# Kernel tuning notes

Hardware: AMD Instinct MI355X
Metric: run time of the kernel (lower is better)

The kernel has to match this reference:

```python
import math
import jax, jax.numpy as jnp
import numpy as np

B, S, D = 4, 2048, 1024
EPS_LN = 1e-5
EPS_MAS = 1e-9


def layernorm(x, g, b):
    m = jnp.mean(x, axis=-1, keepdims=True)
    v = jnp.mean(jnp.square(x - m), axis=-1, keepdims=True)
    return (x - m) * jax.lax.rsqrt(v + EPS_LN) * g + b


def spl(x, proto_w, mu_w, mu_b, gate):
    # match_values = x @ proto^T / sqrt(d);  comp = silu(x @ mu^T + b)
    match = jnp.einsum('bsd,od->bso', x, proto_w) / math.sqrt(x.shape[-1])
    comp = jax.nn.silu(jnp.einsum('bsd,od->bso', x, mu_w) + mu_b)
    return comp, match, gate


def branch(comp, match, gate, passthrough):
    # mas_normalize on the 1-D gate vector (cost), broadcast over [B,S,D]
    cost = gate / (jnp.max(jnp.abs(gate)) + EPS_MAS)
    rl = match - cost
    mrl = jax.nn.relu(rl)
    mask = (rl > 0).astype(comp.dtype)
    return comp * mrl + passthrough * (1.0 - mask)


def causal_attention(q, k, v):
    # num_heads = 1, head_dim = D, is_causal=True
    scale = 1.0 / math.sqrt(q.shape[-1])
    scores = jnp.einsum('bqd,bkd->bqk', q, k) * scale
    causal = jnp.tril(jnp.ones((q.shape[1], k.shape[1]), dtype=bool))
    scores = jnp.where(causal, scores, jnp.asarray(-1e9, scores.dtype))
    p = jax.nn.softmax(scores, axis=-1)
    return jnp.einsum('bqk,bkd->bqd', p, v)


def setup_inputs() -> dict:
    key = jax.random.key(0)
    ks = jax.random.split(key, 16)
    d = D
    std = 0.02
    inp = {
        'x': jax.random.normal(ks[0], (B, S, d), jnp.float32),
        'ln_g': jnp.ones((d,), jnp.float32),
        'ln_b': jnp.zeros((d,), jnp.float32),
    }
    names = ['q', 'k', 'v', 'o']
    for i, n in enumerate(names):
        inp[f'{n}_mu_w'] = std * jax.random.normal(ks[1 + 3 * i], (d, d), jnp.float32)
        inp[f'{n}_mu_b'] = jnp.zeros((d,), jnp.float32)
        inp[f'{n}_proto'] = std * jax.random.normal(ks[2 + 3 * i], (d, d), jnp.float32)
        inp[f'{n}_gate'] = 0.1 * jax.random.normal(ks[3 + 3 * i], (d,), jnp.float32)
    return inp


def reference(x, ln_g, ln_b,
              q_mu_w, q_mu_b, q_proto, q_gate,
              k_mu_w, k_mu_b, k_proto, k_gate,
              v_mu_w, v_mu_b, v_proto, v_gate,
              o_mu_w, o_mu_b, o_proto, o_gate):
    ln1_out = layernorm(x, ln_g, ln_b)

    c_q, mv_q, g_q = spl(ln1_out, q_proto, q_mu_w, q_mu_b, q_gate)
    c_k, mv_k, g_k = spl(ln1_out, k_proto, k_mu_w, k_mu_b, k_gate)
    c_v, mv_v, g_v = spl(ln1_out, v_proto, v_mu_w, v_mu_b, v_gate)

    q = branch(c_q, mv_q, g_q, ln1_out)
    k = branch(c_k, mv_k, g_k, ln1_out)
    v = branch(c_v, mv_v, g_v, ln1_out)

    attn_out = causal_attention(q, k, v)

    c_o, mv_o, g_o = spl(attn_out, o_proto, o_mu_w, o_mu_b, o_gate)
    masked_o = branch(c_o, mv_o, g_o, attn_out)

    x_out = x + masked_o
    return x_out
```

## Files before the change

### kernel.cpp

```cpp
#include <hip/hip_runtime.h>
#include <hip/hip_bf16.h>
#include <cmath>
#include <cstdint>

typedef _Float16 f16;
typedef _Float16 f16x8 __attribute__((ext_vector_type(8)));
typedef float f32x4 __attribute__((ext_vector_type(4)));

#define D_ 1024
#define S_ 2048


__device__ __forceinline__ void gload_lds16(const void* g, void* l) {
  __builtin_amdgcn_global_load_lds(
      (const __attribute__((address_space(1))) void*)(unsigned long long)(uintptr_t)g,
      (__attribute__((address_space(3))) void*)(unsigned int)(uintptr_t)l,
      16, 0, 0);
}

__device__ __forceinline__ void stage_tile(const f16* __restrict__ src, int ld,
                                           f16* lds, int wid, int lane) {
  const int r = (wid << 5) + (lane >> 2);
  const int c = (lane & 3) ^ ((r >> 1) & 3);
  const f16* g0 = src + (size_t)r * ld + (c << 3);
  gload_lds16(g0, lds + (wid << 10));
  gload_lds16(g0 + (size_t)(ld << 4), lds + (wid << 10) + 512);
}

__device__ __forceinline__ int lds_off(int row, int cb) {
  return (row << 5) + ((cb ^ ((row >> 1) & 3)) << 3);
}

__device__ __forceinline__ void split1024(float v, f16& h, f16& l) {
  float s = v * 1024.f;
  h = (f16)s;
  l = (f16)(s - (float)h);
}

__global__ __launch_bounds__(256) void convert_w(
    const float* __restrict__ s0, const float* __restrict__ s1,
    const float* __restrict__ s2, const float* __restrict__ s3,
    const float* __restrict__ s4, const float* __restrict__ s5,
    const float* __restrict__ s6, const float* __restrict__ s7,
    f16* __restrict__ dst) {
  const float* srcs[8] = {s0, s1, s2, s3, s4, s5, s6, s7};
  const float* sp = srcs[blockIdx.y];
  f16* hi = dst + (size_t)blockIdx.y * 2097152;
  f16* lo = hi + 1048576;
  const int i = (blockIdx.x * 256 + threadIdx.x) << 2;
  float4 f = *(const float4*)(sp + i);
  __align__(8) f16 h4[4], l4[4];
  split1024(f.x, h4[0], l4[0]); split1024(f.y, h4[1], l4[1]);
  split1024(f.z, h4[2], l4[2]); split1024(f.w, h4[3], l4[3]);
  *(uint2*)(hi + i) = *(uint2*)h4;
  *(uint2*)(lo + i) = *(uint2*)l4;
}

__global__ __launch_bounds__(256) void cost_k(
    const float* __restrict__ g0, const float* __restrict__ g1,
    const float* __restrict__ g2, const float* __restrict__ g3,
    float* __restrict__ cost) {
  const float* gp = blockIdx.x == 0 ? g0 : blockIdx.x == 1 ? g1
                   : blockIdx.x == 2 ? g2 : g3;
  const int t = threadIdx.x;
  float4 v = *(const float4*)(gp + (t << 2));
  float mx = fmaxf(fmaxf(fabsf(v.x), fabsf(v.y)), fmaxf(fabsf(v.z), fabsf(v.w)));
  for (int o = 32; o; o >>= 1) mx = fmaxf(mx, __shfl_xor(mx, o, 64));
  __shared__ float red[4];
  if ((t & 63) == 0) red[t >> 6] = mx;
  __syncthreads();
  mx = fmaxf(fmaxf(red[0], red[1]), fmaxf(red[2], red[3]));
  const float den = mx + 1e-9f;
  float4 o = {v.x / den, v.y / den, v.z / den, v.w / den};
  *(float4*)(cost + (blockIdx.x << 10) + (t << 2)) = o;
}

__global__ __launch_bounds__(256) void layernorm_k(
    const float* __restrict__ x, const float* __restrict__ g,
    const float* __restrict__ bta, f16* __restrict__ Lh, f16* __restrict__ Ll) {
  const int row = blockIdx.x, t = threadIdx.x;
  const float* xr = x + (size_t)row * D_;
  float4 v = *(const float4*)(xr + (t << 2));
  float s = v.x + v.y + v.z + v.w;
  float q = v.x * v.x + v.y * v.y + v.z * v.z + v.w * v.w;
  for (int o = 32; o; o >>= 1) { s += __shfl_xor(s, o, 64); q += __shfl_xor(q, o, 64); }
  __shared__ float red[8];
  const int wid = t >> 6;
  if ((t & 63) == 0) { red[wid] = s; red[4 + wid] = q; }
  __syncthreads();
  s = red[0] + red[1] + red[2] + red[3];
  q = red[4] + red[5] + red[6] + red[7];
  const float mean = s * (1.f / D_);
  const float var = q * (1.f / D_) - mean * mean;
  const float inv = 1.f / sqrtf(var + 1e-5f);
  float4 gv = *(const float4*)(g + (t << 2));
  float4 bv = *(const float4*)(bta + (t << 2));
  __align__(8) f16 h4[4], l4[4];
  split1024((v.x - mean) * inv * gv.x + bv.x, h4[0], l4[0]);
  split1024((v.y - mean) * inv * gv.y + bv.y, h4[1], l4[1]);
  split1024((v.z - mean) * inv * gv.z + bv.z, h4[2], l4[2]);
  split1024((v.w - mean) * inv * gv.w + bv.w, h4[3], l4[3]);
  const size_t off = (size_t)row * D_ + (t << 2);
  *(uint2*)(Lh + off) = *(uint2*)h4;
  *(uint2*)(Ll + off) = *(uint2*)l4;
}

template <int EPI, int MUP>
__global__ __launch_bounds__(256, 2) void dual_gemm_branch(
    const f16* __restrict__ Ah, const f16* __restrict__ Al,
    const f16* __restrict__ Wph, const f16* __restrict__ Wpl,
    const f16* __restrict__ Wmh, const f16* __restrict__ Wml,
    const float* __restrict__ bias, const float* __restrict__ cost,
    const f16* __restrict__ passh, const f16* __restrict__ passl,
    const float* __restrict__ xres, f16* __restrict__ outh,
    f16* __restrict__ outl, float* __restrict__ outf) {
  __shared__ __align__(16) f16 lAh[4096], lAl[4096], lPh[4096], lPl[4096],
      lMh[4096], lMl[4096];
  const int tid = threadIdx.x, wid = tid >> 6, lane = tid & 63;
  const int row0 = blockIdx.x << 7, col0 = blockIdx.y << 7;
  const int wr = (wid >> 1) << 6, wc = (wid & 1) << 6;
  const int arow = lane & 15, cb = lane >> 4;
  const f32x4 zero = {0.f, 0.f, 0.f, 0.f};
  f32x4 accP[4][4], accM[4][4];
#pragma unroll
  for (int m = 0; m < 4; ++m)
#pragma unroll
    for (int n = 0; n < 4; ++n) { accP[m][n] = zero; accM[m][n] = zero; }
  const f16* Ahb = Ah + (size_t)row0 * D_;
  const f16* Alb = Al + (size_t)row0 * D_;
  const f16* Phb = Wph + (size_t)col0 * D_;
  const f16* Plb = Wpl + (size_t)col0 * D_;
  const f16* Mhb = Wmh + (size_t)col0 * D_;
  const f16* Mlb = Wml + (size_t)col0 * D_;
  for (int k = 0; k < D_; k += 32) {
    stage_tile(Ahb + k, D_, lAh, wid, lane);
    stage_tile(Alb + k, D_, lAl, wid, lane);
    stage_tile(Phb + k, D_, lPh, wid, lane);
    stage_tile(Plb + k, D_, lPl, wid, lane);
    stage_tile(Mhb + k, D_, lMh, wid, lane);
    stage_tile(Mlb + k, D_, lMl, wid, lane);
    __syncthreads();
    f16x8 bph[4], bpl[4], bmh[4], bml[4];
#pragma unroll
    for (int n = 0; n < 4; ++n) {
      const int bo = lds_off(wc + n * 16 + arow, cb);
      bph[n] = *(const f16x8*)&lPh[bo];
      bpl[n] = *(const f16x8*)&lPl[bo];
      bmh[n] = *(const f16x8*)&lMh[bo];
      bml[n] = *(const f16x8*)&lMl[bo];
    }
#pragma unroll
    for (int m = 0; m < 4; ++m) {
      const int ao = lds_off(wr + m * 16 + arow, cb);
      f16x8 ah = *(const f16x8*)&lAh[ao];
      f16x8 al = *(const f16x8*)&lAl[ao];
#pragma unroll
      for (int n = 0; n < 4; ++n) {
        accP[m][n] = __builtin_amdgcn_mfma_f32_16x16x32_f16(ah, bph[n], accP[m][n], 0, 0, 0);
        accP[m][n] = __builtin_amdgcn_mfma_f32_16x16x32_f16(ah, bpl[n], accP[m][n], 0, 0, 0);
        accP[m][n] = __builtin_amdgcn_mfma_f32_16x16x32_f16(al, bph[n], accP[m][n], 0, 0, 0);
        accM[m][n] = __builtin_amdgcn_mfma_f32_16x16x32_f16(ah, bmh[n], accM[m][n], 0, 0, 0);
        accM[m][n] = __builtin_amdgcn_mfma_f32_16x16x32_f16(ah, bml[n], accM[m][n], 0, 0, 0);
        if (MUP == 3)
          accM[m][n] = __builtin_amdgcn_mfma_f32_16x16x32_f16(al, bmh[n], accM[m][n], 0, 0, 0);
      }
    }
    __syncthreads();
  }
#pragma unroll
  for (int m = 0; m < 4; ++m) {
    const int rb = row0 + wr + m * 16 + ((lane >> 4) << 2);
#pragma unroll
    for (int n = 0; n < 4; ++n) {
      const int col = col0 + wc + n * 16 + (lane & 15);
      const float cb2 = cost[col], bb = bias[col];
#pragma unroll
      for (int j = 0; j < 4; ++j) {
        const size_t off = (size_t)(rb + j) * D_ + col;
        const float match = accP[m][n][j] * (1.f / 33554432.f);
        const float pre = accM[m][n][j] * (1.f / 1048576.f) + bb;
        const float comp = pre / (1.f + expf(-pre));
        const float rl = match - cb2;
        float ov;
        if (rl > 0.f) ov = comp * rl;
        else ov = ((float)passh[off] + (float)passl[off]) * (1.f / 1024.f);
        if (EPI == 0) {
          f16 h, l; split1024(ov, h, l);
          outh[off] = h; outl[off] = l;
        } else {
          outf[off] = xres[off] + ov;
        }
      }
    }
  }
}

__global__ __launch_bounds__(256) void transpose_v(
    const f16* __restrict__ Vh, const f16* __restrict__ Vl,
    f16* __restrict__ VTh, f16* __restrict__ VTl) {
  const int iz = blockIdx.z, b = iz & 3;
  const f16* src = (iz >> 2) ? Vl : Vh;
  f16* dst = (iz >> 2) ? VTl : VTh;
  const int d0 = blockIdx.x << 6, s0 = blockIdx.y << 6;
  __shared__ f16 tl[64][65];
  const int c = threadIdx.x & 63, r4 = threadIdx.x >> 6;
  const f16* vb = src + (size_t)b * S_ * D_;
#pragma unroll
  for (int i = 0; i < 16; ++i) {
    const int sr = (r4 << 4) + i;
    tl[sr][c] = vb[(size_t)(s0 + sr) * D_ + d0 + c];
  }
  __syncthreads();
  f16* db = dst + (size_t)b * D_ * S_;
#pragma unroll
  for (int i = 0; i < 16; ++i) {
    const int dr = (r4 << 4) + i;
    db[(size_t)(d0 + dr) * S_ + s0 + c] = tl[c][dr];
  }
}

__global__ __launch_bounds__(256, 2) void scores_gemm(
    const f16* __restrict__ Qh, const f16* __restrict__ Ql,
    const f16* __restrict__ Kh, const f16* __restrict__ Kl,
    float* __restrict__ SC) {
  const int rt = blockIdx.x, ct = blockIdx.y, b = blockIdx.z;
  if (ct > rt) return;
  __shared__ __align__(16) f16 lQh[4096], lQl[4096], lKh[4096], lKl[4096];
  const int tid = threadIdx.x, wid = tid >> 6, lane = tid & 63;
  const int row0 = rt << 7, col0 = ct << 7;
  const int wr = (wid >> 1) << 6, wc = (wid & 1) << 6;
  const int arow = lane & 15, cb = lane >> 4;
  const f32x4 zero = {0.f, 0.f, 0.f, 0.f};
  f32x4 acc[4][4];
#pragma unroll
  for (int m = 0; m < 4; ++m)
#pragma unroll
    for (int n = 0; n < 4; ++n) acc[m][n] = zero;
  const f16* Qhb = Qh + ((size_t)b * S_ + row0) * D_;
  const f16* Qlb = Ql + ((size_t)b * S_ + row0) * D_;
  const f16* Khb = Kh + ((size_t)b * S_ + col0) * D_;
  const f16* Klb = Kl + ((size_t)b * S_ + col0) * D_;
  for (int k = 0; k < D_; k += 32) {
    stage_tile(Qhb + k, D_, lQh, wid, lane);
    stage_tile(Qlb + k, D_, lQl, wid, lane);
    stage_tile(Khb + k, D_, lKh, wid, lane);
    stage_tile(Klb + k, D_, lKl, wid, lane);
    __syncthreads();
    f16x8 bh[4], bl[4];
#pragma unroll
    for (int n = 0; n < 4; ++n) {
      const int bo = lds_off(wc + n * 16 + arow, cb);
      bh[n] = *(const f16x8*)&lKh[bo];
      bl[n] = *(const f16x8*)&lKl[bo];
    }
#pragma unroll
    for (int m = 0; m < 4; ++m) {
      const int ao = lds_off(wr + m * 16 + arow, cb);
      f16x8 ah = *(const f16x8*)&lQh[ao];
      f16x8 al = *(const f16x8*)&lQl[ao];
#pragma unroll
      for (int n = 0; n < 4; ++n) {
        acc[m][n] = __builtin_amdgcn_mfma_f32_16x16x32_f16(ah, bh[n], acc[m][n], 0, 0, 0);
        acc[m][n] = __builtin_amdgcn_mfma_f32_16x16x32_f16(ah, bl[n], acc[m][n], 0, 0, 0);
        acc[m][n] = __builtin_amdgcn_mfma_f32_16x16x32_f16(al, bh[n], acc[m][n], 0, 0, 0);
      }
    }
    __syncthreads();
  }
  float* scb = SC + (size_t)b * S_ * S_;
#pragma unroll
  for (int m = 0; m < 4; ++m) {
    const int rb = row0 + wr + m * 16 + ((lane >> 4) << 2);
#pragma unroll
    for (int n = 0; n < 4; ++n) {
      const int col = col0 + wc + n * 16 + (lane & 15);
#pragma unroll
      for (int j = 0; j < 4; ++j)
        scb[(size_t)(rb + j) * S_ + col] = acc[m][n][j] * (1.f / 33554432.f);
    }
  }
}

__global__ __launch_bounds__(256) void softmax_rows(float* __restrict__ SC) {
  const int r = blockIdx.x;
  const int s = r & 2047;
  float* rowf = SC + (size_t)r * S_;
  const int t = threadIdx.x, c0 = t << 3;
  float f[8];
  float4 u0 = *(const float4*)(rowf + c0);
  float4 u1 = *(const float4*)(rowf + c0 + 4);
  f[0] = u0.x; f[1] = u0.y; f[2] = u0.z; f[3] = u0.w;
  f[4] = u1.x; f[5] = u1.y; f[6] = u1.z; f[7] = u1.w;
  float mx = -3.0e38f;
#pragma unroll
  for (int j = 0; j < 8; ++j)
    if (c0 + j <= s) mx = fmaxf(mx, f[j]);
  for (int o = 32; o; o >>= 1) mx = fmaxf(mx, __shfl_xor(mx, o, 64));
  __shared__ float red[8];
  const int wid = t >> 6;
  if ((t & 63) == 0) red[wid] = mx;
  __syncthreads();
  mx = fmaxf(fmaxf(red[0], red[1]), fmaxf(red[2], red[3]));
  float e[8];
  float sum = 0.f;
#pragma unroll
  for (int j = 0; j < 8; ++j) {
    e[j] = (c0 + j <= s) ? expf(f[j] - mx) : 0.f;
    sum += e[j];
  }
  for (int o = 32; o; o >>= 1) sum += __shfl_xor(sum, o, 64);
  if ((t & 63) == 0) red[4 + wid] = sum;
  __syncthreads();
  sum = red[4] + red[5] + red[6] + red[7];
  f16* rowh = (f16*)rowf;
  __align__(16) f16 ph[8], pl[8];
#pragma unroll
  for (int j = 0; j < 8; ++j) {
    float p = (e[j] / sum) * 2048.f;
    ph[j] = (f16)p;
    pl[j] = (f16)(p - (float)ph[j]);
  }
  *(uint4*)(rowh + c0) = *(uint4*)ph;
  *(uint4*)(rowh + 2048 + c0) = *(uint4*)pl;
}

__global__ __launch_bounds__(256, 2) void pv_gemm(
    const f16* __restrict__ P, const f16* __restrict__ VTh,
    const f16* __restrict__ VTl, f16* __restrict__ Ath, f16* __restrict__ Atl) {
  const int rt = blockIdx.x, ct = blockIdx.y, b = blockIdx.z;
  __shared__ __align__(16) f16 lPh[4096], lPl[4096], lVh[4096], lVl[4096];
  const int tid = threadIdx.x, wid = tid >> 6, lane = tid & 63;
  const int row0 = rt << 7, col0 = ct << 7;
  const int wr = (wid >> 1) << 6, wc = (wid & 1) << 6;
  const int arow = lane & 15, cb = lane >> 4;
  const f32x4 zero = {0.f, 0.f, 0.f, 0.f};
  f32x4 acc[4][4];
#pragma unroll
  for (int m = 0; m < 4; ++m)
#pragma unroll
    for (int n = 0; n < 4; ++n) acc[m][n] = zero;
  const f16* Pb = P + ((size_t)b * S_ + row0) * 4096;
  const f16* Vhb = VTh + (size_t)b * D_ * S_ + (size_t)col0 * S_;
  const f16* Vlb = VTl + (size_t)b * D_ * S_ + (size_t)col0 * S_;
  const int kend = (rt + 1) << 7;
  for (int k = 0; k < kend; k += 32) {
    stage_tile(Pb + k, 4096, lPh, wid, lane);
    stage_tile(Pb + 2048 + k, 4096, lPl, wid, lane);
    stage_tile(Vhb + k, S_, lVh, wid, lane);
    stage_tile(Vlb + k, S_, lVl, wid, lane);
    __syncthreads();
    f16x8 bh[4], bl[4];
#pragma unroll
    for (int n = 0; n < 4; ++n) {
      const int bo = lds_off(wc + n * 16 + arow, cb);
      bh[n] = *(const f16x8*)&lVh[bo];
      bl[n] = *(const f16x8*)&lVl[bo];
    }
#pragma unroll
    for (int m = 0; m < 4; ++m) {
      const int ao = lds_off(wr + m * 16 + arow, cb);
      f16x8 ah = *(const f16x8*)&lPh[ao];
      f16x8 al = *(const f16x8*)&lPl[ao];
#pragma unroll
      for (int n = 0; n < 4; ++n) {
        acc[m][n] = __builtin_amdgcn_mfma_f32_16x16x32_f16(ah, bh[n], acc[m][n], 0, 0, 0);
        acc[m][n] = __builtin_amdgcn_mfma_f32_16x16x32_f16(ah, bl[n], acc[m][n], 0, 0, 0);
        acc[m][n] = __builtin_amdgcn_mfma_f32_16x16x32_f16(al, bh[n], acc[m][n], 0, 0, 0);
      }
    }
    __syncthreads();
  }
#pragma unroll
  for (int m = 0; m < 4; ++m) {
    const int rb = row0 + wr + m * 16 + ((lane >> 4) << 2);
#pragma unroll
    for (int n = 0; n < 4; ++n) {
      const int col = col0 + wc + n * 16 + (lane & 15);
#pragma unroll
      for (int j = 0; j < 4; ++j) {
        const float at = acc[m][n][j] * (1.f / 2097152.f);
        const size_t off = ((size_t)b * S_ + rb + j) * D_ + col;
        f16 h, l; split1024(at, h, l);
        Ath[off] = h; Atl[off] = l;
      }
    }
  }
}

extern "C" void kernel_launch(void* const* d_in, const int* in_sizes, int n_in,
                              void* d_out, int out_size, void* d_ws, size_t ws_size,
                              hipStream_t stream) {
  (void)in_sizes; (void)n_in; (void)out_size; (void)ws_size;
  const float* x      = (const float*)d_in[0];
  const float* ln_g   = (const float*)d_in[1];
  const float* ln_b   = (const float*)d_in[2];
  const float* q_mu_w = (const float*)d_in[3];
  const float* q_mu_b = (const float*)d_in[4];
  const float* q_pro  = (const float*)d_in[5];
  const float* q_gate = (const float*)d_in[6];
  const float* k_mu_w = (const float*)d_in[7];
  const float* k_mu_b = (const float*)d_in[8];
  const float* k_pro  = (const float*)d_in[9];
  const float* k_gate = (const float*)d_in[10];
  const float* v_mu_w = (const float*)d_in[11];
  const float* v_mu_b = (const float*)d_in[12];
  const float* v_pro  = (const float*)d_in[13];
  const float* v_gate = (const float*)d_in[14];
  const float* o_mu_w = (const float*)d_in[15];
  const float* o_mu_b = (const float*)d_in[16];
  const float* o_pro  = (const float*)d_in[17];
  const float* o_gate = (const float*)d_in[18];

  char* w = (char*)d_ws;
  f16* WB = (f16*)w;
  const size_t WS = 2097152;
  f16* Lh  = (f16*)(w + 33554432);
  f16* Ll  = (f16*)(w + 50331648);
  f16* Qh  = (f16*)(w + 67108864);
  f16* Ql  = (f16*)(w + 83886080);
  f16* Kh  = (f16*)(w + 100663296);
  f16* Kl  = (f16*)(w + 117440512);
  f16* VTh = (f16*)(w + 134217728);
  f16* VTl = (f16*)(w + 150994944);
  float* SC = (float*)(w + 167772160);
  float* COST = (float*)(w + 234881024);
  f16* Vh = (f16*)SC;
  f16* Vl = (f16*)(w + 184549376);
  f16* Ath = Qh;  f16* Atl = Ql;

  convert_w<<<dim3(1024, 8), 256, 0, stream>>>(
      q_pro, q_mu_w, k_pro, k_mu_w, v_pro, v_mu_w, o_pro, o_mu_w, WB);
  cost_k<<<4, 256, 0, stream>>>(q_gate, k_gate, v_gate, o_gate, COST);
  layernorm_k<<<8192, 256, 0, stream>>>(x, ln_g, ln_b, Lh, Ll);

  dual_gemm_branch<0, 3><<<dim3(64, 8), 256, 0, stream>>>(
      Lh, Ll, WB, WB + 1048576, WB + WS, WB + WS + 1048576,
      q_mu_b, COST, Lh, Ll, nullptr, Qh, Ql, nullptr);
  dual_gemm_branch<0, 3><<<dim3(64, 8), 256, 0, stream>>>(
      Lh, Ll, WB + 2 * WS, WB + 2 * WS + 1048576, WB + 3 * WS, WB + 3 * WS + 1048576,
      k_mu_b, COST + 1024, Lh, Ll, nullptr, Kh, Kl, nullptr);
  dual_gemm_branch<0, 3><<<dim3(64, 8), 256, 0, stream>>>(
      Lh, Ll, WB + 4 * WS, WB + 4 * WS + 1048576, WB + 5 * WS, WB + 5 * WS + 1048576,
      v_mu_b, COST + 2048, Lh, Ll, nullptr, Vh, Vl, nullptr);

  transpose_v<<<dim3(16, 32, 8), 256, 0, stream>>>(Vh, Vl, VTh, VTl);
  scores_gemm<<<dim3(16, 16, 4), 256, 0, stream>>>(Qh, Ql, Kh, Kl, SC);
  softmax_rows<<<8192, 256, 0, stream>>>(SC);
  pv_gemm<<<dim3(16, 8, 4), 256, 0, stream>>>((const f16*)SC, VTh, VTl, Ath, Atl);

  dual_gemm_branch<1, 2><<<dim3(64, 8), 256, 0, stream>>>(
      Ath, Atl, WB + 6 * WS, WB + 6 * WS + 1048576, WB + 7 * WS, WB + 7 * WS + 1048576,
      o_mu_b, COST + 3072, Ath, Atl, x, nullptr, nullptr, (float*)d_out);
}
```

Measured before the change: 708.3 us.

## Double-buffer dual GEMM LDS loads and enlarge block tile to 256 rows

```diff
diff --git a/kernel.cpp b/kernel.cpp
--- a/kernel.cpp
+++ b/kernel.cpp
@@ -16,6 +16,16 @@
       (const __attribute__((address_space(1))) void*)(unsigned long long)(uintptr_t)g,
       (__attribute__((address_space(3))) void*)(unsigned int)(uintptr_t)l,
       16, 0, 0);
+}
+
+__device__ __forceinline__ int lds_off(int row, int cb) {
+  return (row << 5) + ((cb ^ ((row >> 1) & 3)) << 3);
+}
+
+__device__ __forceinline__ void split1024(float v, f16& h, f16& l) {
+  float s = v * 1024.f;
+  h = (f16)s;
+  l = (f16)(s - (float)h);
 }
 
 __device__ __forceinline__ void stage_tile(const f16* __restrict__ src, int ld,
@@ -25,16 +35,6 @@
   const f16* g0 = src + (size_t)r * ld + (c << 3);
   gload_lds16(g0, lds + (wid << 10));
   gload_lds16(g0 + (size_t)(ld << 4), lds + (wid << 10) + 512);
-}
-
-__device__ __forceinline__ int lds_off(int row, int cb) {
-  return (row << 5) + ((cb ^ ((row >> 1) & 3)) << 3);
-}
-
-__device__ __forceinline__ void split1024(float v, f16& h, f16& l) {
-  float s = v * 1024.f;
-  h = (f16)s;
-  l = (f16)(s - (float)h);
 }
 
 __global__ __launch_bounds__(256) void convert_w(
@@ -106,7 +106,7 @@
 }
 
 template <int EPI, int MUP>
-__global__ __launch_bounds__(256, 2) void dual_gemm_branch(
+__global__ __launch_bounds__(512, 1) void dual_gemm_v2(
     const f16* __restrict__ Ah, const f16* __restrict__ Al,
     const f16* __restrict__ Wph, const f16* __restrict__ Wpl,
     const f16* __restrict__ Wmh, const f16* __restrict__ Wml,
@@ -114,59 +114,93 @@
     const f16* __restrict__ passh, const f16* __restrict__ passl,
     const float* __restrict__ xres, f16* __restrict__ outh,
     f16* __restrict__ outl, float* __restrict__ outf) {
-  __shared__ __align__(16) f16 lAh[4096], lAl[4096], lPh[4096], lPl[4096],
-      lMh[4096], lMl[4096];
+  __shared__ __align__(16) f16 smem[65536];
   const int tid = threadIdx.x, wid = tid >> 6, lane = tid & 63;
-  const int row0 = blockIdx.x << 7, col0 = blockIdx.y << 7;
+  const int row0 = blockIdx.x << 8, col0 = blockIdx.y << 7;
   const int wr = (wid >> 1) << 6, wc = (wid & 1) << 6;
-  const int arow = lane & 15, cb = lane >> 4;
+  const int arow = lane & 15, cbk = lane >> 4;
+
+  const int sr = tid >> 2;
+  const int sc = ((tid & 3) ^ ((sr >> 1) & 3)) << 3;
+  const int wbase = wid << 9;
+
+  const f16* pA0 = Ah + (size_t)(row0 + sr) * D_ + sc;
+  const f16* pA1 = Ah + (size_t)(row0 + 128 + sr) * D_ + sc;
+  const f16* pL0 = Al + (size_t)(row0 + sr) * D_ + sc;
+  const f16* pL1 = Al + (size_t)(row0 + 128 + sr) * D_ + sc;
+  const f16* pPh = Wph + (size_t)(col0 + sr) * D_ + sc;
+  const f16* pPl = Wpl + (size_t)(col0 + sr) * D_ + sc;
+  const f16* pMh = Wmh + (size_t)(col0 + sr) * D_ + sc;
+  const f16* pMl = Wml + (size_t)(col0 + sr) * D_ + sc;
+
   const f32x4 zero = {0.f, 0.f, 0.f, 0.f};
   f32x4 accP[4][4], accM[4][4];
 #pragma unroll
   for (int m = 0; m < 4; ++m)
 #pragma unroll
     for (int n = 0; n < 4; ++n) { accP[m][n] = zero; accM[m][n] = zero; }
-  const f16* Ahb = Ah + (size_t)row0 * D_;
-  const f16* Alb = Al + (size_t)row0 * D_;
-  const f16* Phb = Wph + (size_t)col0 * D_;
-  const f16* Plb = Wpl + (size_t)col0 * D_;
-  const f16* Mhb = Wmh + (size_t)col0 * D_;
-  const f16* Mlb = Wml + (size_t)col0 * D_;
-  for (int k = 0; k < D_; k += 32) {
-    stage_tile(Ahb + k, D_, lAh, wid, lane);
-    stage_tile(Alb + k, D_, lAl, wid, lane);
-    stage_tile(Phb + k, D_, lPh, wid, lane);
-    stage_tile(Plb + k, D_, lPl, wid, lane);
-    stage_tile(Mhb + k, D_, lMh, wid, lane);
-    stage_tile(Mlb + k, D_, lMl, wid, lane);
-    __syncthreads();
-    f16x8 bph[4], bpl[4], bmh[4], bml[4];
-#pragma unroll
-    for (int n = 0; n < 4; ++n) {
-      const int bo = lds_off(wc + n * 16 + arow, cb);
-      bph[n] = *(const f16x8*)&lPh[bo];
-      bpl[n] = *(const f16x8*)&lPl[bo];
-      bmh[n] = *(const f16x8*)&lMh[bo];
-      bml[n] = *(const f16x8*)&lMl[bo];
-    }
+
+  auto STAGE = [&](f16* buf, int k) {
+    gload_lds16(pA0 + k, buf + wbase);
+    gload_lds16(pA1 + k, buf + 4096 + wbase);
+    gload_lds16(pL0 + k, buf + 8192 + wbase);
+    gload_lds16(pL1 + k, buf + 12288 + wbase);
+    gload_lds16(pPh + k, buf + 16384 + wbase);
+    gload_lds16(pPl + k, buf + 20480 + wbase);
+    gload_lds16(pMh + k, buf + 24576 + wbase);
+    gload_lds16(pMl + k, buf + 28672 + wbase);
+  };
+
+  auto COMPUTE = [&](const f16* buf) {
+    const f16* bAh = buf;
+    const f16* bAl = buf + 8192;
+    const f16* bPh = buf + 16384;
+    const f16* bPl = buf + 20480;
+    const f16* bMh = buf + 24576;
+    const f16* bMl = buf + 28672;
+    f16x8 ah[4], al[4];
 #pragma unroll
     for (int m = 0; m < 4; ++m) {
-      const int ao = lds_off(wr + m * 16 + arow, cb);
-      f16x8 ah = *(const f16x8*)&lAh[ao];
-      f16x8 al = *(const f16x8*)&lAl[ao];
-#pragma unroll
-      for (int n = 0; n < 4; ++n) {
-        accP[m][n] = __builtin_amdgcn_mfma_f32_16x16x32_f16(ah, bph[n], accP[m][n], 0, 0, 0);
-        accP[m][n] = __builtin_amdgcn_mfma_f32_16x16x32_f16(ah, bpl[n], accP[m][n], 0, 0, 0);
-        accP[m][n] = __builtin_amdgcn_mfma_f32_16x16x32_f16(al, bph[n], accP[m][n], 0, 0, 0);
-        accM[m][n] = __builtin_amdgcn_mfma_f32_16x16x32_f16(ah, bmh[n], accM[m][n], 0, 0, 0);
-        accM[m][n] = __builtin_amdgcn_mfma_f32_16x16x32_f16(ah, bml[n], accM[m][n], 0, 0, 0);
+      const int ao = lds_off(wr + m * 16 + arow, cbk);
+      ah[m] = *(const f16x8*)&bAh[ao];
+      al[m] = *(const f16x8*)&bAl[ao];
+    }
+#pragma unroll
+    for (int n = 0; n < 4; ++n) {
+      const int bo = lds_off(wc + n * 16 + arow, cbk);
+      f16x8 bph = *(const f16x8*)&bPh[bo];
+      f16x8 bpl = *(const f16x8*)&bPl[bo];
+      f16x8 bmh = *(const f16x8*)&bMh[bo];
+      f16x8 bml = *(const f16x8*)&bMl[bo];
+#pragma unroll
+      for (int m = 0; m < 4; ++m) {
+        accP[m][n] = __builtin_amdgcn_mfma_f32_16x16x32_f16(ah[m], bph, accP[m][n], 0, 0, 0);
+        accP[m][n] = __builtin_amdgcn_mfma_f32_16x16x32_f16(ah[m], bpl, accP[m][n], 0, 0, 0);
+        accP[m][n] = __builtin_amdgcn_mfma_f32_16x16x32_f16(al[m], bph, accP[m][n], 0, 0, 0);
+        accM[m][n] = __builtin_amdgcn_mfma_f32_16x16x32_f16(ah[m], bmh, accM[m][n], 0, 0, 0);
+        accM[m][n] = __builtin_amdgcn_mfma_f32_16x16x32_f16(ah[m], bml, accM[m][n], 0, 0, 0);
         if (MUP == 3)
-          accM[m][n] = __builtin_amdgcn_mfma_f32_16x16x32_f16(al, bmh[n], accM[m][n], 0, 0, 0);
+          accM[m][n] = __builtin_amdgcn_mfma_f32_16x16x32_f16(al[m], bmh, accM[m][n], 0, 0, 0);
       }
     }
-    __syncthreads();
-  }
+  };
+
+  STAGE(smem, 0);
+  int cur = 0;
+  for (int t = 0; t < 31; ++t) {
+    STAGE(smem + ((cur ^ 1) << 15), (t + 1) << 5);
+    asm volatile("s_waitcnt vmcnt(8)\n\ts_barrier" ::: "memory");
+    __builtin_amdgcn_s_setprio(1);
+    COMPUTE(smem + (cur << 15));
+    __builtin_amdgcn_s_setprio(0);
+    asm volatile("s_waitcnt lgkmcnt(0)\n\ts_barrier" ::: "memory");
+    cur ^= 1;
+  }
+  asm volatile("s_waitcnt vmcnt(0)\n\ts_barrier" ::: "memory");
+  __builtin_amdgcn_s_setprio(1);
+  COMPUTE(smem + (cur << 15));
+  __builtin_amdgcn_s_setprio(0);
+
 #pragma unroll
   for (int m = 0; m < 4; ++m) {
     const int rb = row0 + wr + m * 16 + ((lane >> 4) << 2);
@@ -433,13 +467,13 @@
   cost_k<<<4, 256, 0, stream>>>(q_gate, k_gate, v_gate, o_gate, COST);
   layernorm_k<<<8192, 256, 0, stream>>>(x, ln_g, ln_b, Lh, Ll);
 
-  dual_gemm_branch<0, 3><<<dim3(64, 8), 256, 0, stream>>>(
+  dual_gemm_v2<0, 3><<<dim3(32, 8), 512, 0, stream>>>(
       Lh, Ll, WB, WB + 1048576, WB + WS, WB + WS + 1048576,
       q_mu_b, COST, Lh, Ll, nullptr, Qh, Ql, nullptr);
-  dual_gemm_branch<0, 3><<<dim3(64, 8), 256, 0, stream>>>(
+  dual_gemm_v2<0, 3><<<dim3(32, 8), 512, 0, stream>>>(
       Lh, Ll, WB + 2 * WS, WB + 2 * WS + 1048576, WB + 3 * WS, WB + 3 * WS + 1048576,
       k_mu_b, COST + 1024, Lh, Ll, nullptr, Kh, Kl, nullptr);
-  dual_gemm_branch<0, 3><<<dim3(64, 8), 256, 0, stream>>>(
+  dual_gemm_v2<0, 3><<<dim3(32, 8), 512, 0, stream>>>(
       Lh, Ll, WB + 4 * WS, WB + 4 * WS + 1048576, WB + 5 * WS, WB + 5 * WS + 1048576,
       v_mu_b, COST + 2048, Lh, Ll, nullptr, Vh, Vl, nullptr);
 
@@ -448,7 +482,7 @@
   softmax_rows<<<8192, 256, 0, stream>>>(SC);
   pv_gemm<<<dim3(16, 8, 4), 256, 0, stream>>>((const f16*)SC, VTh, VTl, Ath, Atl);
 
-  dual_gemm_branch<1, 2><<<dim3(64, 8), 256, 0, stream>>>(
+  dual_gemm_v2<1, 2><<<dim3(32, 8), 512, 0, stream>>>(
       Ath, Atl, WB + 6 * WS, WB + 6 * WS + 1048576, WB + 7 * WS, WB + 7 * WS + 1048576,
       o_mu_b, COST + 3072, Ath, Atl, x, nullptr, nullptr, (float*)d_out);
 }
```

Measured after the change: 712.3 us. No clear change (+0.6%).
